# Kernel optimization log

Hardware: AMD Instinct MI355X
Metric: run time of the kernel (lower is better)

## Reference

```python
import jax, jax.numpy as jnp
import numpy as np

B, S, F_DIM, FILT = 4096, 41, 128, 128
EPS_BN = 1e-5
EPS_SQ = 1e-21


def squash(v):
    n = jnp.linalg.norm(v, axis=-1, keepdims=True)
    return (1.0 - 1.0 / (jnp.exp(n) + EPS_SQ)) * (v / (n + EPS_SQ))


def position_linear(x, Wstack, bstack, window):
    # x: [B,S,F]; Wstack: [S, window*F, FILT]; bstack: [S, FILT]
    p = window // 2
    Bq, Sq, Fq = x.shape
    xp = jnp.pad(x, ((0, 0), (p, p), (0, 0)))
    idx = jnp.arange(Sq)[:, None] + jnp.arange(window)[None, :]  # [S, window]
    xw = xp[:, idx, :].reshape(Bq, Sq, window * Fq)
    return jax.nn.relu(jnp.einsum('bsf,sfo->bso', xw, Wstack) + bstack[None])


def batchnorm(x, g, b, axes):
    mu = jnp.mean(x, axis=axes, keepdims=True)
    var = jnp.var(x, axis=axes, keepdims=True)
    shape = [1] * x.ndim
    shape[1] = x.shape[1]
    return (x - mu) * jax.lax.rsqrt(var + EPS_BN) * g.reshape(shape) + b.reshape(shape)


def conv1d(x, w, groups=1):
    # x: [N,C,L], w: [O, C//groups, K], padding same (k=3, pad=1)
    return jax.lax.conv_general_dilated(
        x, w, window_strides=(1,), padding=[(1, 1)],
        dimension_numbers=('NCH', 'OIH', 'NCH'), feature_group_count=groups)


def setup_inputs() -> dict:
    key = jax.random.key(0)
    ks = jax.random.split(key, 16)
    sc = lambda fan_in: 1.0 / np.sqrt(fan_in)
    d = {}
    d['x'] = jax.random.randint(ks[0], (B, S), 0, 4, dtype=jnp.int32)
    d['emb'] = jax.random.normal(ks[1], (4, F_DIM), dtype=jnp.float32)
    for i, w in enumerate([3, 5, 7]):
        fin = w * F_DIM
        d[f'W{w}'] = jax.random.uniform(ks[2 + i], (S, fin, FILT), jnp.float32, -sc(fin), sc(fin))
        d[f'b{w}'] = jnp.zeros((S, FILT), jnp.float32)
    d['conv1_w'] = jax.random.uniform(ks[5], (64, 41, 3), jnp.float32, -sc(41 * 3), sc(41 * 3))
    d['conv1_b'] = jnp.zeros((64,), jnp.float32)
    d['bn_g'] = jnp.ones((64,), jnp.float32)
    d['bn_b'] = jnp.zeros((64,), jnp.float32)
    d['caps_w'] = jax.random.uniform(ks[6], (64, 32, 3), jnp.float32, -sc(32 * 3), sc(32 * 3))
    d['caps_b'] = jnp.zeros((64,), jnp.float32)
    d['route_W'] = jax.random.normal(ks[7], (2, 64, F_DIM), jnp.float32)
    d['route_b'] = jnp.zeros((2, 64, 1), jnp.float32)
    d['fc1_w'] = jax.random.uniform(ks[8], (F_DIM, 64), jnp.float32, -sc(F_DIM), sc(F_DIM))
    d['bn1_g'] = jnp.ones((2,), jnp.float32)
    d['bn1_b'] = jnp.zeros((2,), jnp.float32)
    d['fc2_w'] = jax.random.uniform(ks[9], (64, 32), jnp.float32, -sc(64), sc(64))
    d['bn2_g'] = jnp.ones((2,), jnp.float32)
    d['bn2_b'] = jnp.zeros((2,), jnp.float32)
    d['fc3_w'] = jax.random.uniform(ks[10], (32, 1), jnp.float32, -sc(32), sc(32))
    return d


def reference(x, emb, W3, b3, W5, b5, W7, b7, conv1_w, conv1_b, bn_g, bn_b,
              caps_w, caps_b, route_W, route_b,
              fc1_w, bn1_g, bn1_b, fc2_w, bn2_g, bn2_b, fc3_w):
    h = emb[x]                                    # [B,41,128]
    h = position_linear(h, W3, b3, 3)
    h = position_linear(h, W5, b5, 5)
    h = position_linear(h, W7, b7, 7)             # [B,41,128]
    h = conv1d(h, conv1_w) + conv1_b[None, :, None]  # [B,64,128]
    h = jax.nn.relu(batchnorm(h, bn_g, bn_b, axes=(0, 2)))
    h = conv1d(h, caps_w, groups=2) + caps_b[None, :, None]
    h = squash(h)                                 # [B,64,128]
    # Routing layer
    u = h[:, None, :, :] * route_W[None]          # [B,2,64,128]
    c = jnp.sum(u * u, axis=-1, keepdims=True) / jnp.sqrt(128.0)  # [B,2,64,1]
    c = jax.nn.softmax(c, axis=-1)                # softmax over size-1 axis -> ones
    c = c + route_b[None]
    s = squash(jnp.sum(u * c, axis=-2))           # [B,2,128]
    # FC head
    pair = s[:, :, None, :] + s[:, None, :, :]    # [B,2,2,128]
    y = jnp.max(pair, axis=1)                     # [B,2,128]
    y = jax.nn.relu(batchnorm(y @ fc1_w, bn1_g, bn1_b, axes=(0, 2)))
    y = jax.nn.relu(batchnorm(y @ fc2_w, bn2_g, bn2_b, axes=(0, 2)))
    y = jax.nn.sigmoid(y @ fc3_w)                 # [B,2,1]
    return jnp.max(y, axis=1)                     # [B,1]
```

## Files before the change

### kernel.cpp

```cpp
#include <hip/hip_runtime.h>
#include <cstdint>

typedef unsigned short u16;
typedef unsigned int   u32;
typedef __attribute__((ext_vector_type(8))) short bf16x8;
typedef __attribute__((ext_vector_type(4))) float f32x4;

#define DEVFN static __device__ __forceinline__

constexpr int B  = 4096;
constexpr int SQ = 41;

DEVFN float bf2f(u16 v) { return __uint_as_float(((u32)v) << 16); }
DEVFN u16 f2bf(float f) {
  u32 u = __float_as_uint(f);
  u += 0x7fffu + ((u >> 16) & 1u);
  return (u16)(u >> 16);
}
DEVFN u32 pack2(float a, float b) { return (u32)f2bf(a) | ((u32)f2bf(b) << 16); }

DEVFN void gload16(const void* g, void* l) {
  __builtin_amdgcn_global_load_lds(
      (const __attribute__((address_space(1))) unsigned int*)g,
      (__attribute__((address_space(3))) unsigned int*)l, 16, 0, 0);
}

__global__ void k_pack(const float* __restrict__ cw, const float* __restrict__ cpw,
                       const float* __restrict__ rW, const float* __restrict__ rb,
                       u16* __restrict__ wpk, u16* __restrict__ cpk,
                       u16* __restrict__ rwp) {
  int i = blockIdx.x * 256 + threadIdx.x;
  if (i < 12288) {
    int tt = i >> 12, rem = i & 4095, o = rem >> 6, c = rem & 63;
    float v = (c < 41) ? cw[(o * 41 + c) * 3 + tt] : 0.f;
    wpk[(tt * 64 + o) * 64 + (c ^ ((o & 7) << 3))] = f2bf(v);
  } else if (i < 18432) {
    int k = i - 12288;
    int tt = k >> 11, rem = k & 2047, o = rem >> 5, c = rem & 31;
    cpk[(tt * 64 + o) * 32 + (c ^ ((o & 3) << 3))] = f2bf(cpw[(o * 32 + c) * 3 + tt]);
  } else if (i < 34816) {
    int k = i - 18432;
    rwp[k] = f2bf(rW[k] * (1.f + rb[k >> 7]));
  }
}

__global__ void k_combo(const int* __restrict__ x, int* __restrict__ combo) {
  int i = blockIdx.x * 256 + threadIdx.x;
  if (i >= B * SQ) return;
  int b = i / SQ, s = i - b * SQ;
  const int* xb = x + b * SQ;
  int d0 = (s > 0) ? xb[s - 1] : 4;
  int d1 = xb[s];
  int d2 = (s < SQ - 1) ? xb[s + 1] : 4;
  combo[i] = d0 * 25 + d1 * 5 + d2;
}

__global__ void k_gmat(const float* __restrict__ emb, const float* __restrict__ W3,
                       float* __restrict__ G) {
  int s = blockIdx.x / 3, ww = blockIdx.x % 3;
  int o = threadIdx.x;
  const float* Ws = W3 + ((size_t)s * 384 + ww * 128) * 128;
  float a0 = 0.f, a1 = 0.f, a2 = 0.f, a3 = 0.f;
  for (int f = 0; f < 128; ++f) {
    float wg = Ws[(size_t)f * 128 + o];
    a0 = fmaf(emb[f], wg, a0);
    a1 = fmaf(emb[128 + f], wg, a1);
    a2 = fmaf(emb[256 + f], wg, a2);
    a3 = fmaf(emb[384 + f], wg, a3);
  }
  float* Gp = G + ((size_t)(s * 3 + ww) * 5) * 128 + o;
  Gp[0] = a0; Gp[128] = a1; Gp[256] = a2; Gp[384] = a3; Gp[512] = 0.f;
}

__global__ void k_t1(const float* __restrict__ G, const float* __restrict__ b3,
                     float* __restrict__ t1T) {
  int i = blockIdx.x * 256 + threadIdx.x;
  if (i >= SQ * 128 * 125) return;
  int v = i % 125, so = i / 125;
  int s = so >> 7, o = so & 127;
  int d0 = v / 25, r = v % 25;
  int d1 = r / 5, d2 = r % 5;
  float acc = b3[so]
      + G[((size_t)(s * 3 + 0) * 5 + d0) * 128 + o]
      + G[((size_t)(s * 3 + 1) * 5 + d1) * 128 + o]
      + G[((size_t)(s * 3 + 2) * 5 + d2) * 128 + o];
  t1T[i] = fmaxf(acc, 0.f);
}

__global__ __launch_bounds__(128) void k_t2(const float* __restrict__ t1T,
                                            const float* __restrict__ W5,
                                            u16* __restrict__ t2) {
  int bx = blockIdx.x;
  int s = bx / 25; int r = bx % 25;
  int ww = r / 5;  int vt = (r % 5) * 25;
  int o = threadIdx.x;
  int t = s + ww - 2;
  u16* dst = t2 + ((size_t)(s * 5 + ww) * 125 + vt) * 128 + o;
  if (t < 0 || t >= SQ) {
    #pragma unroll
    for (int v = 0; v < 25; ++v) dst[(size_t)v * 128] = 0;
    return;
  }
  float acc[25];
  #pragma unroll
  for (int v = 0; v < 25; ++v) acc[v] = 0.f;
  const float* Ws = W5 + ((size_t)s * 640 + ww * 128) * 128;
  const float* tp = t1T + (size_t)t * 128 * 125 + vt;
  for (int f = 0; f < 128; ++f) {
    float wg = Ws[(size_t)f * 128 + o];
    #pragma unroll
    for (int v = 0; v < 25; ++v) acc[v] = fmaf(tp[f * 125 + v], wg, acc[v]);
  }
  #pragma unroll
  for (int v = 0; v < 25; ++v) dst[(size_t)v * 128] = f2bf(acc[v]);
}

__global__ __launch_bounds__(256) void k_h2(const u16* __restrict__ t2,
                                            const int* __restrict__ combo,
                                            const float* __restrict__ b5,
                                            u16* __restrict__ h2) {
  const int i = blockIdx.x * 256 + threadIdx.x;
  const int o8 = (i & 15) * 8;
  const int rid = i >> 4;
  const int s = rid >> 12, b = rid & 4095;
  float acc[8];
  {
    float4 b0 = *reinterpret_cast<const float4*>(b5 + s * 128 + o8);
    float4 b1 = *reinterpret_cast<const float4*>(b5 + s * 128 + o8 + 4);
    acc[0] = b0.x; acc[1] = b0.y; acc[2] = b0.z; acc[3] = b0.w;
    acc[4] = b1.x; acc[5] = b1.y; acc[6] = b1.z; acc[7] = b1.w;
  }
  const int* cb = combo + b * SQ;
  #pragma unroll
  for (int ww = 0; ww < 5; ++ww) {
    const int t = s + ww - 2;
    if (0 <= t && t < SQ) {
      const int c = cb[t];
      uint4 raw = *reinterpret_cast<const uint4*>(
          t2 + ((size_t)(s * 5 + ww) * 125 + c) * 128 + o8);
      acc[0] += __uint_as_float(raw.x << 16);
      acc[1] += __uint_as_float(raw.x & 0xffff0000u);
      acc[2] += __uint_as_float(raw.y << 16);
      acc[3] += __uint_as_float(raw.y & 0xffff0000u);
      acc[4] += __uint_as_float(raw.z << 16);
      acc[5] += __uint_as_float(raw.z & 0xffff0000u);
      acc[6] += __uint_as_float(raw.w << 16);
      acc[7] += __uint_as_float(raw.w & 0xffff0000u);
    }
  }
  uint4 pk;
  pk.x = pack2(fmaxf(acc[0], 0.f), fmaxf(acc[1], 0.f));
  pk.y = pack2(fmaxf(acc[2], 0.f), fmaxf(acc[3], 0.f));
  pk.z = pack2(fmaxf(acc[4], 0.f), fmaxf(acc[5], 0.f));
  pk.w = pack2(fmaxf(acc[6], 0.f), fmaxf(acc[7], 0.f));
  *reinterpret_cast<uint4*>(h2 + ((size_t)b * SQ + s) * 128 + o8) = pk;
}

__global__ __launch_bounds__(256) void k_w7t(const float* __restrict__ W7,
                                             u16* __restrict__ w7t) {
  __shared__ float tile[64][65];
  const int s = blockIdx.z;
  const int k0 = blockIdx.x * 64;
  const int o0 = blockIdx.y * 64;
  const int t = threadIdx.x;
  #pragma unroll
  for (int i = 0; i < 16; ++i) {
    int idx = t + i * 256;
    int kl = idx >> 6, ol = idx & 63;
    tile[kl][ol] = W7[((size_t)s * 896 + k0 + kl) * 128 + o0 + ol];
  }
  __syncthreads();
  #pragma unroll
  for (int i = 0; i < 16; ++i) {
    int idx = t + i * 256;
    int ol = idx >> 6, kl = idx & 63;
    w7t[((size_t)s * 128 + o0 + ol) * 896 + k0 + kl] = f2bf(tile[kl][ol]);
  }
}

__global__ __launch_bounds__(256) void k_gemm7_mfma(const u16* __restrict__ h2,
                                                    const u16* __restrict__ w7t,
                                                    const float* __restrict__ b7,
                                                    u16* __restrict__ h3) {
  __shared__ u16 As[2][8192];
  __shared__ u16 Bs[2][8192];
  const int s  = blockIdx.y;
  const int b0 = blockIdx.x * 128;
  const int t  = threadIdx.x;
  const int lane = t & 63, w = t >> 6;
  const int wr = w >> 1, wc = w & 1;
  const int lcol = lane & 15, qk = lane >> 4;

  f32x4 acc[4][4];
  #pragma unroll
  for (int i = 0; i < 4; ++i)
    #pragma unroll
    for (int j = 0; j < 4; ++j) acc[i][j] = (f32x4){0.f, 0.f, 0.f, 0.f};

  const u16* wbase = w7t + (size_t)s * 128 * 896;

  auto stage = [&](int kt, int bi) -> int {
    const int k0 = kt * 64;
    const int ww = k0 >> 7, tr = s + ww - 3, kf0 = k0 & 127;
    int issued = 0;
    if (0 <= tr && tr < SQ) {
      #pragma unroll
      for (int it = 0; it < 4; ++it) {
        const int L = it * 4096 + t * 16;
        const int r = L >> 7;
        const int g = (L >> 4) & 7;
        const int gs = g ^ (r & 7);
        gload16(h2 + ((size_t)(b0 + r) * SQ + tr) * 128 + kf0 + gs * 8,
                (char*)As[bi] + it * 4096 + w * 1024);
      }
      issued += 4;
    } else {
      #pragma unroll
      for (int it = 0; it < 4; ++it)
        *reinterpret_cast<uint4*>((char*)As[bi] + it * 4096 + t * 16) =
            make_uint4(0u, 0u, 0u, 0u);
    }
    #pragma unroll
    for (int it = 0; it < 4; ++it) {
      const int L = it * 4096 + t * 16;
      const int o = L >> 7;
      const int g = (L >> 4) & 7;
      const int gs = g ^ (o & 7);
      gload16(wbase + (size_t)o * 896 + k0 + gs * 8,
              (char*)Bs[bi] + it * 4096 + w * 1024);
    }
    return issued + 4;
  };

  stage(0, 0);

  for (int kt = 0; kt < 14; ++kt) {
    const int cur = kt & 1;
    int ni = 0;
    if (kt < 13) ni = stage(kt + 1, cur ^ 1);
    if (ni == 8)      asm volatile("s_waitcnt vmcnt(8) lgkmcnt(0)" ::: "memory");
    else if (ni == 4) asm volatile("s_waitcnt vmcnt(4) lgkmcnt(0)" ::: "memory");
    else              asm volatile("s_waitcnt vmcnt(0) lgkmcnt(0)" ::: "memory");
    __builtin_amdgcn_sched_barrier(0);
    __builtin_amdgcn_s_barrier();
    __builtin_amdgcn_sched_barrier(0);

    const u16* Ac = As[cur];
    const u16* Bc = Bs[cur];
    #pragma unroll
    for (int kk = 0; kk < 2; ++kk) {
      const int gk = kk * 4 + qk;
      bf16x8 av[4], bv[4];
      #pragma unroll
      for (int m = 0; m < 4; ++m) {
        const int zr = wr * 64 + m * 16 + lcol;
        av[m] = *reinterpret_cast<const bf16x8*>(Ac + zr * 64 + ((gk ^ (zr & 7)) << 3));
      }
      #pragma unroll
      for (int n = 0; n < 4; ++n) {
        const int br = wc * 64 + n * 16 + lcol;
        bv[n] = *reinterpret_cast<const bf16x8*>(Bc + br * 64 + ((gk ^ (br & 7)) << 3));
      }
      #pragma unroll
      for (int m = 0; m < 4; ++m)
        #pragma unroll
        for (int n = 0; n < 4; ++n)
          acc[m][n] = __builtin_amdgcn_mfma_f32_16x16x32_bf16(av[m], bv[n], acc[m][n], 0, 0, 0);
    }
    __builtin_amdgcn_sched_barrier(0);
    __builtin_amdgcn_s_barrier();
  }

  const int rq = (lane >> 4) * 4;
  #pragma unroll
  for (int n = 0; n < 4; ++n) {
    const int o = wc * 64 + n * 16 + lcol;
    const float bias = b7[s * 128 + o];
    #pragma unroll
    for (int m = 0; m < 4; ++m) {
      #pragma unroll
      for (int rg = 0; rg < 4; ++rg) {
        const int row = b0 + wr * 64 + m * 16 + rq + rg;
        h3[((size_t)row * SQ + s) * 128 + o] = f2bf(fmaxf(acc[m][n][rg] + bias, 0.f));
      }
    }
  }
}

__global__ __launch_bounds__(256) void k_conv1(const u16* __restrict__ h3,
                                               const u16* __restrict__ wpk,
                                               const float* __restrict__ cb,
                                               u16* __restrict__ c1T,
                                               float2* __restrict__ part) {
  __shared__ u16 zs[6144];
  __shared__ u16 zt[130 * 64];
  __shared__ u16 wl[3 * 64 * 64];
  __shared__ float2 red[4][64];
  const int b = blockIdx.x;
  const int t = threadIdx.x;
  const int lane = t & 63, wv = t >> 6;

  const u16* src = h3 + (size_t)b * (SQ * 128);
  #pragma unroll
  for (int it = 0; it < 3; ++it)
    gload16(src + ((size_t)it * 256 + t) * 8, (char*)zs + it * 4096 + wv * 1024);
  #pragma unroll
  for (int it = 0; it < 6; ++it)
    gload16(wpk + ((size_t)it * 256 + t) * 8, (char*)wl + it * 4096 + wv * 1024);

  if (t < 64) zt[t] = 0;
  else if (t < 128) zt[129 * 64 + t - 64] = 0;
  __syncthreads();

  {
    const int l = t & 127, jb = (t >> 7) * 32;
    const int sw = ((l + 1) & 7) << 3;
    u16* dst = zt + (l + 1) * 64;
    #pragma unroll
    for (int j = 0; j < 32; ++j) {
      int c = (jb + j + l) & 63;
      dst[c ^ sw] = (c < 41) ? zs[c * 128 + l] : (u16)0;
    }
  }
  __syncthreads();

  f32x4 acc[2][4];
  #pragma unroll
  for (int m = 0; m < 2; ++m)
    #pragma unroll
    for (int n = 0; n < 4; ++n) acc[m][n] = (f32x4){0.f, 0.f, 0.f, 0.f};
  const int r = lane & 15, kq = (lane >> 4) * 8;

  #pragma unroll
  for (int tt = 0; tt < 3; ++tt) {
    #pragma unroll
    for (int kk = 0; kk < 2; ++kk) {
      const int kof = kk * 32 + kq;
      bf16x8 av[2], bv[4];
      #pragma unroll
      for (int m = 0; m < 2; ++m) {
        const int zr = wv * 32 + m * 16 + r + tt;
        av[m] = *reinterpret_cast<const bf16x8*>(zt + zr * 64 + (kof ^ ((zr & 7) << 3)));
      }
      #pragma unroll
      for (int n = 0; n < 4; ++n) {
        const int o = n * 16 + r;
        bv[n] = *reinterpret_cast<const bf16x8*>(wl + (tt * 64 + o) * 64 + (kof ^ ((o & 7) << 3)));
      }
      #pragma unroll
      for (int m = 0; m < 2; ++m)
        #pragma unroll
        for (int n = 0; n < 4; ++n)
          acc[m][n] = __builtin_amdgcn_mfma_f32_16x16x32_bf16(av[m], bv[n], acc[m][n], 0, 0, 0);
    }
  }

  const int q = lane >> 4;
  u16* outb = c1T + (size_t)b * 8192;
  #pragma unroll
  for (int n = 0; n < 4; ++n) {
    const int o = n * 16 + r;
    const float bias = cb[o];
    float s1 = 0.f, s2 = 0.f;
    #pragma unroll
    for (int m = 0; m < 2; ++m) {
      #pragma unroll
      for (int rg = 0; rg < 4; ++rg) {
        float v = acc[m][n][rg] + bias;
        s1 += v; s2 += v * v;
        outb[(wv * 32 + m * 16 + q * 4 + rg) * 64 + o] = f2bf(v);
      }
    }
    s1 += __shfl_xor(s1, 16); s1 += __shfl_xor(s1, 32);
    s2 += __shfl_xor(s2, 16); s2 += __shfl_xor(s2, 32);
    if (lane < 16) red[wv][n * 16 + lane] = make_float2(s1, s2);
  }
  __syncthreads();
  if (t < 64) {
    float S = red[0][t].x + red[1][t].x + red[2][t].x + red[3][t].x;
    float Q = red[0][t].y + red[1][t].y + red[2][t].y + red[3][t].y;
    part[(size_t)t * B + b] = make_float2(S, Q);
  }
}

__global__ void k_bnfin(const float2* __restrict__ part, const float* __restrict__ g,
                        const float* __restrict__ bb, float* __restrict__ scale,
                        float* __restrict__ shift) {
  int o = blockIdx.x;
  float s = 0.f, q = 0.f;
  for (int i = threadIdx.x; i < B; i += 256) {
    float2 p = part[(size_t)o * B + i];
    s += p.x; q += p.y;
  }
  #pragma unroll
  for (int off = 32; off; off >>= 1) { s += __shfl_down(s, off); q += __shfl_down(q, off); }
  __shared__ float rs[4], rq[4];
  int wv = threadIdx.x >> 6, ln = threadIdx.x & 63;
  if (ln == 0) { rs[wv] = s; rq[wv] = q; }
  __syncthreads();
  if (threadIdx.x == 0) {
    float S = rs[0] + rs[1] + rs[2] + rs[3];
    float Q = rq[0] + rq[1] + rq[2] + rq[3];
    const float n = (float)B * 128.f;
    float mu = S / n, var = Q / n - mu * mu;
    float sc = g[o] * rsqrtf(var + 1e-5f);
    scale[o] = sc; shift[o] = bb[o] - mu * sc;
  }
}

constexpr int NB = 8;
__global__ __launch_bounds__(256) void k_caps(const u16* __restrict__ c1T,
                                              const float* __restrict__ scale,
                                              const float* __restrict__ shift,
                                              const u16* __restrict__ cpk,
                                              const float* __restrict__ cpb,
                                              const u16* __restrict__ rwp,
                                              const float* __restrict__ f1,
                                              float* __restrict__ y1) {
  __shared__ u16 zt[130 * 64];
  __shared__ u16 wl[3 * 64 * 32];
  __shared__ float f1l[128 * 64];
  __shared__ float red[4][64];
  __shared__ float fl[64];
  __shared__ float sc_s[64], sh_s[64];
  __shared__ float red2[4][2];
  __shared__ float yl[2][128];
  __shared__ float pt[128];
  const int b0 = blockIdx.x * NB;
  const int t = threadIdx.x;
  const int lane = t & 63, wv = t >> 6;
  const int r = lane & 15, kq = (lane >> 4) * 8, q = lane >> 4;

  #pragma unroll
  for (int it = 0; it < 3; ++it)
    gload16(cpk + ((size_t)it * 256 + t) * 8, (char*)wl + it * 4096 + wv * 1024);
  #pragma unroll
  for (int it = 0; it < 8; ++it)
    gload16(f1 + ((size_t)it * 256 + t) * 4, (char*)f1l + it * 4096 + wv * 1024);
  if (t < 64) { sc_s[t] = scale[t]; sh_s[t] = shift[t]; }
  if (t < 64) zt[t] = 0;
  else if (t < 128) zt[129 * 64 + t - 64] = 0;

  uint4 raw[4], rawn[4];
  {
    const u16* src = c1T + (size_t)b0 * 8192;
    #pragma unroll
    for (int p = 0; p < 4; ++p)
      raw[p] = *reinterpret_cast<const uint4*>(src + ((size_t)t + p * 256) * 8);
  }

  for (int i = 0; i < NB; ++i) {
    const int b = b0 + i;
    __syncthreads();

    #pragma unroll
    for (int p = 0; p < 4; ++p) {
      int idx = t + p * 256;
      int l = idx >> 3, c0 = (idx & 7) * 8;
      float vv[8];
      vv[0] = __uint_as_float(raw[p].x << 16); vv[1] = __uint_as_float(raw[p].x & 0xffff0000u);
      vv[2] = __uint_as_float(raw[p].y << 16); vv[3] = __uint_as_float(raw[p].y & 0xffff0000u);
      vv[4] = __uint_as_float(raw[p].z << 16); vv[5] = __uint_as_float(raw[p].z & 0xffff0000u);
      vv[6] = __uint_as_float(raw[p].w << 16); vv[7] = __uint_as_float(raw[p].w & 0xffff0000u);
      float a0 = fmaxf(fmaf(vv[0], sc_s[c0 + 0], sh_s[c0 + 0]), 0.f);
      float a1 = fmaxf(fmaf(vv[1], sc_s[c0 + 1], sh_s[c0 + 1]), 0.f);
      float a2 = fmaxf(fmaf(vv[2], sc_s[c0 + 2], sh_s[c0 + 2]), 0.f);
      float a3 = fmaxf(fmaf(vv[3], sc_s[c0 + 3], sh_s[c0 + 3]), 0.f);
      float a4 = fmaxf(fmaf(vv[4], sc_s[c0 + 4], sh_s[c0 + 4]), 0.f);
      float a5 = fmaxf(fmaf(vv[5], sc_s[c0 + 5], sh_s[c0 + 5]), 0.f);
      float a6 = fmaxf(fmaf(vv[6], sc_s[c0 + 6], sh_s[c0 + 6]), 0.f);
      float a7 = fmaxf(fmaf(vv[7], sc_s[c0 + 7], sh_s[c0 + 7]), 0.f);
      uint4 pk;
      pk.x = pack2(a0, a1); pk.y = pack2(a2, a3);
      pk.z = pack2(a4, a5); pk.w = pack2(a6, a7);
      *reinterpret_cast<uint4*>(zt + (l + 1) * 64 + (c0 ^ (((l + 1) & 7) << 3))) = pk;
    }
    if (i + 1 < NB) {
      const u16* srcn = c1T + (size_t)(b + 1) * 8192;
      #pragma unroll
      for (int p = 0; p < 4; ++p)
        rawn[p] = *reinterpret_cast<const uint4*>(srcn + ((size_t)t + p * 256) * 8);
    }
    __syncthreads();

    f32x4 acc[2][4];
    #pragma unroll
    for (int m = 0; m < 2; ++m)
      #pragma unroll
      for (int n = 0; n < 4; ++n) acc[m][n] = (f32x4){0.f, 0.f, 0.f, 0.f};
    #pragma unroll
    for (int tt = 0; tt < 3; ++tt) {
      bf16x8 av[2][2], bv[4];
      #pragma unroll
      for (int m = 0; m < 2; ++m) {
        const int zr = wv * 32 + m * 16 + r + tt;
        const int sw = (zr & 7) << 3;
        av[m][0] = *reinterpret_cast<const bf16x8*>(zt + zr * 64 + (kq ^ sw));
        av[m][1] = *reinterpret_cast<const bf16x8*>(zt + zr * 64 + ((32 + kq) ^ sw));
      }
      #pragma unroll
      for (int n = 0; n < 4; ++n) {
        const int o = n * 16 + r;
        bv[n] = *reinterpret_cast<const bf16x8*>(wl + (tt * 64 + o) * 32 + (kq ^ ((o & 3) << 3)));
      }
      #pragma unroll
      for (int m = 0; m < 2; ++m)
        #pragma unroll
        for (int n = 0; n < 4; ++n)
          acc[m][n] = __builtin_amdgcn_mfma_f32_16x16x32_bf16(av[m][n >> 1], bv[n], acc[m][n], 0, 0, 0);
    }

    #pragma unroll
    for (int n = 0; n < 4; ++n) {
      const int o = n * 16 + r;
      const float bias = cpb[o];
      float s2 = 0.f;
      #pragma unroll
      for (int m = 0; m < 2; ++m) {
        #pragma unroll
        for (int rg = 0; rg < 4; ++rg) {
          float v = acc[m][n][rg] + bias;
          acc[m][n][rg] = v;
          s2 += v * v;
        }
      }
      s2 += __shfl_xor(s2, 16); s2 += __shfl_xor(s2, 32);
      if (lane < 16) red[wv][n * 16 + lane] = s2;
    }
    __syncthreads();
    if (t < 64) {
      float S = red[0][t] + red[1][t] + red[2][t] + red[3][t];
      float nn = sqrtf(S);
      fl[t] = (1.f - 1.f / (expf(nn) + 1e-21f)) / (nn + 1e-21f);
    }
    __syncthreads();

    float s0[2][4], s1[2][4];
    #pragma unroll
    for (int m = 0; m < 2; ++m)
      #pragma unroll
      for (int rg = 0; rg < 4; ++rg) { s0[m][rg] = 0.f; s1[m][rg] = 0.f; }
    #pragma unroll
    for (int n = 0; n < 4; ++n) {
      const int o = n * 16 + r;
      const float fact = fl[o];
      #pragma unroll
      for (int m = 0; m < 2; ++m) {
        const int l0 = wv * 32 + m * 16 + q * 4;
        uint2 rw0 = *reinterpret_cast<const uint2*>(rwp + (size_t)o * 128 + l0);
        uint2 rw1 = *reinterpret_cast<const uint2*>(rwp + (size_t)(64 + o) * 128 + l0);
        #pragma unroll
        for (int rg = 0; rg < 4; ++rg) {
          float v = acc[m][n][rg] * fact;
          u32 w0w = (rg < 2) ? rw0.x : rw0.y;
          u32 w1w = (rg < 2) ? rw1.x : rw1.y;
          float w0 = __uint_as_float((rg & 1) ? (w0w & 0xffff0000u) : (w0w << 16));
          float w1 = __uint_as_float((rg & 1) ? (w1w & 0xffff0000u) : (w1w << 16));
          s0[m][rg] = fmaf(v, w0, s0[m][rg]);
          s1[m][rg] = fmaf(v, w1, s1[m][rg]);
        }
      }
    }
    #pragma unroll
    for (int m = 0; m < 2; ++m)
      #pragma unroll
      for (int rg = 0; rg < 4; ++rg) {
        #pragma unroll
        for (int off = 1; off <= 8; off <<= 1) {
          s0[m][rg] += __shfl_xor(s0[m][rg], off);
          s1[m][rg] += __shfl_xor(s1[m][rg], off);
        }
      }
    float n0 = 0.f, n1 = 0.f;
    #pragma unroll
    for (int m = 0; m < 2; ++m)
      #pragma unroll
      for (int rg = 0; rg < 4; ++rg) {
        n0 = fmaf(s0[m][rg], s0[m][rg], n0);
        n1 = fmaf(s1[m][rg], s1[m][rg], n1);
      }
    n0 += __shfl_xor(n0, 16); n0 += __shfl_xor(n0, 32);
    n1 += __shfl_xor(n1, 16); n1 += __shfl_xor(n1, 32);
    if (lane == 0) { red2[wv][0] = n0; red2[wv][1] = n1; }
    __syncthreads();
    {
      float t0 = red2[0][0] + red2[1][0] + red2[2][0] + red2[3][0];
      float t1 = red2[0][1] + red2[1][1] + red2[2][1] + red2[3][1];
      float nn0 = sqrtf(t0), nn1 = sqrtf(t1);
      float fa0 = (1.f - 1.f / (expf(nn0) + 1e-21f)) / (nn0 + 1e-21f);
      float fa1 = (1.f - 1.f / (expf(nn1) + 1e-21f)) / (nn1 + 1e-21f);
      if (r == 0) {
        #pragma unroll
        for (int m = 0; m < 2; ++m)
          #pragma unroll
          for (int rg = 0; rg < 4; ++rg) {
            float v0 = s0[m][rg] * fa0, v1 = s1[m][rg] * fa1;
            float mx = fmaxf(v0, v1);
            int l = wv * 32 + m * 16 + q * 4 + rg;
            yl[0][l] = v0 + mx;
            yl[1][l] = v1 + mx;
          }
      }
    }
    __syncthreads();

    {
      const int h = t >> 7, idx = t & 127;
      const int jj = idx >> 6, qq = idx & 63;
      float a = 0.f;
      const float* yrow = &yl[jj][h * 64];
      const float* frow = f1l + (h * 64) * 64 + qq;
      #pragma unroll 8
      for (int tt = 0; tt < 64; ++tt)
        a = fmaf(yrow[tt], frow[tt * 64], a);
      if (h == 1) pt[idx] = a;
      __syncthreads();
      if (h == 0)
        y1[((size_t)b * 2 + jj) * 64 + qq] = a + pt[idx];
    }

    #pragma unroll
    for (int p = 0; p < 4; ++p) raw[p] = rawn[p];
  }
}

__global__ __launch_bounds__(256) void k_bnstat_part(const float* __restrict__ y,
                                                     float2* __restrict__ pp,
                                                     int perShift) {
  const int jj = blockIdx.y;
  const int per = 1 << perShift;
  const int n4 = (B << perShift) >> 2;
  const int p4shift = perShift - 2;
  const int p4mask = (per >> 2) - 1;
  float s = 0.f, q = 0.f;
  for (int i = blockIdx.x * 256 + threadIdx.x; i < n4; i += 64 * 256) {
    int bI = i >> p4shift, c4 = (i & p4mask) * 4;
    float4 v = *reinterpret_cast<const float4*>(
        y + (size_t)bI * (per * 2) + jj * per + c4);
    s += v.x + v.y + v.z + v.w;
    q += v.x * v.x + v.y * v.y + v.z * v.z + v.w * v.w;
  }
  #pragma unroll
  for (int off = 32; off; off >>= 1) { s += __shfl_down(s, off); q += __shfl_down(q, off); }
  __shared__ float rs[4], rq[4];
  int wv = threadIdx.x >> 6, ln = threadIdx.x & 63;
  if (ln == 0) { rs[wv] = s; rq[wv] = q; }
  __syncthreads();
  if (threadIdx.x == 0)
    pp[jj * 64 + blockIdx.x] =
        make_float2(rs[0] + rs[1] + rs[2] + rs[3], rq[0] + rq[1] + rq[2] + rq[3]);
}

__global__ void k_bnstat_fin(const float2* __restrict__ pp, const float* __restrict__ g,
                             const float* __restrict__ bb, float* __restrict__ scale,
                             float* __restrict__ shift, int perShift) {
  const int jj = blockIdx.x;
  float2 p = pp[jj * 64 + threadIdx.x];
  float s = p.x, q = p.y;
  #pragma unroll
  for (int off = 32; off; off >>= 1) { s += __shfl_down(s, off); q += __shfl_down(q, off); }
  if (threadIdx.x == 0) {
    float fn = (float)(B << perShift);
    float mu = s / fn, var = q / fn - mu * mu;
    float sc = g[jj] * rsqrtf(var + 1e-5f);
    scale[jj] = sc; shift[jj] = bb[jj] - mu * sc;
  }
}

__global__ void k_fc2(const float* __restrict__ y1, const float* __restrict__ sc1,
                      const float* __restrict__ sh1, const float* __restrict__ f2,
                      float* __restrict__ y2) {
  int t = threadIdx.x;
  int b = blockIdx.x * 4 + (t >> 6);
  int jj = (t >> 5) & 1, r = t & 31;
  float sc = sc1[jj], sh = sh1[jj];
  const float* yb = y1 + (size_t)b * 128 + jj * 64;
  float acc = 0.f;
  for (int q = 0; q < 64; ++q) {
    float v = fmaxf(fmaf(yb[q], sc, sh), 0.f);
    acc = fmaf(v, f2[q * 32 + r], acc);
  }
  y2[(size_t)b * 64 + jj * 32 + r] = acc;
}

__global__ void k_head(const float* __restrict__ y2, const float* __restrict__ sc2,
                       const float* __restrict__ sh2, const float* __restrict__ f3,
                       float* __restrict__ out) {
  int b = blockIdx.x * 256 + threadIdx.x;
  if (b >= B) return;
  const float* yb = y2 + (size_t)b * 64;
  float c0 = sc2[0], d0 = sh2[0], c1v = sc2[1], d1 = sh2[1];
  float a0 = 0.f, a1 = 0.f;
  for (int r = 0; r < 32; ++r) {
    float w = f3[r];
    a0 = fmaf(fmaxf(fmaf(yb[r], c0, d0), 0.f), w, a0);
    a1 = fmaf(fmaxf(fmaf(yb[32 + r], c1v, d1), 0.f), w, a1);
  }
  float s0 = 1.f / (1.f + expf(-a0));
  float s1 = 1.f / (1.f + expf(-a1));
  out[b] = fmaxf(s0, s1);
}

constexpr size_t SZ_H2    = (size_t)B * SQ * 128 * 2;
constexpr size_t SZ_C1    = (size_t)B * 64 * 128 * 2;
constexpr size_t OFF_H2   = 0;
constexpr size_t OFF_H3   = SZ_H2;
constexpr size_t R1       = 2 * SZ_H2;
constexpr size_t OFF_G    = R1;
constexpr size_t OFF_T1   = OFF_G + 314880;
constexpr size_t OFF_T2   = OFF_T1 + 2624000;
constexpr size_t OFF_CMB  = OFF_T2 + 6560000;
constexpr size_t OFF_W7T  = OFF_CMB + 671744;
constexpr size_t OFF_C1   = R1;
constexpr size_t R2       = R1 + SZ_C1;
constexpr size_t OFF_PART = R2;
constexpr size_t OFF_Y1   = OFF_PART + 2097152;
constexpr size_t OFF_Y2   = OFF_Y1 + 2097152;
constexpr size_t OFF_SM   = OFF_Y2 + 1048576;
constexpr size_t OFF_BNP  = OFF_SM + 1024;
constexpr size_t OFF_WPK  = OFF_BNP + 1024;
constexpr size_t OFF_CPK  = OFF_WPK + 24576;
constexpr size_t OFF_RWP  = OFF_CPK + 12288;

extern "C" void kernel_launch(void* const* d_in, const int* in_sizes, int n_in,
                              void* d_out, int out_size, void* d_ws, size_t ws_size,
                              hipStream_t stream) {
  const int*   x   = (const int*)d_in[0];
  const float* emb = (const float*)d_in[1];
  const float* W3  = (const float*)d_in[2];
  const float* b3  = (const float*)d_in[3];
  const float* W5  = (const float*)d_in[4];
  const float* b5  = (const float*)d_in[5];
  const float* W7  = (const float*)d_in[6];
  const float* b7  = (const float*)d_in[7];
  const float* c1w = (const float*)d_in[8];
  const float* c1b = (const float*)d_in[9];
  const float* bng = (const float*)d_in[10];
  const float* bnb = (const float*)d_in[11];
  const float* cpw = (const float*)d_in[12];
  const float* cpb = (const float*)d_in[13];
  const float* rW  = (const float*)d_in[14];
  const float* rb  = (const float*)d_in[15];
  const float* f1  = (const float*)d_in[16];
  const float* g1  = (const float*)d_in[17];
  const float* bb1 = (const float*)d_in[18];
  const float* f2  = (const float*)d_in[19];
  const float* g2  = (const float*)d_in[20];
  const float* bb2 = (const float*)d_in[21];
  const float* f3  = (const float*)d_in[22];

  char* wsb = (char*)d_ws;
  u16*    h2p   = (u16*)(wsb + OFF_H2);
  u16*    h3p   = (u16*)(wsb + OFF_H3);
  float*  Gp    = (float*)(wsb + OFF_G);
  float*  t1p   = (float*)(wsb + OFF_T1);
  u16*    t2p   = (u16*)(wsb + OFF_T2);
  int*    cmbp  = (int*)(wsb + OFF_CMB);
  u16*    w7tp  = (u16*)(wsb + OFF_W7T);
  u16*    c1p   = (u16*)(wsb + OFF_C1);
  float2* partp = (float2*)(wsb + OFF_PART);
  float*  y1p   = (float*)(wsb + OFF_Y1);
  float*  y2p   = (float*)(wsb + OFF_Y2);
  float*  scp   = (float*)(wsb + OFF_SM);
  float*  shp   = scp + 64;
  float*  sc1p  = shp + 64;
  float*  sh1p  = sc1p + 2;
  float*  sc2p  = sh1p + 2;
  float*  sh2p  = sc2p + 2;
  float2* bnpp  = (float2*)(wsb + OFF_BNP);
  u16*    wpkp  = (u16*)(wsb + OFF_WPK);
  u16*    cpkp  = (u16*)(wsb + OFF_CPK);
  u16*    rwpp  = (u16*)(wsb + OFF_RWP);

  k_pack<<<136, 256, 0, stream>>>(c1w, cpw, rW, rb, wpkp, cpkp, rwpp);
  k_combo<<<(B * SQ + 255) / 256, 256, 0, stream>>>(x, cmbp);
  k_w7t<<<dim3(14, 2, SQ), 256, 0, stream>>>(W7, w7tp);
  k_gmat<<<SQ * 3, 128, 0, stream>>>(emb, W3, Gp);
  k_t1<<<(SQ * 128 * 125 + 255) / 256, 256, 0, stream>>>(Gp, b3, t1p);
  k_t2<<<SQ * 25, 128, 0, stream>>>(t1p, W5, t2p);
  k_h2<<<(B * SQ * 16) / 256, 256, 0, stream>>>(t2p, cmbp, b5, h2p);
  k_gemm7_mfma<<<dim3(32, SQ), 256, 0, stream>>>(h2p, w7tp, b7, h3p);
  k_conv1<<<B, 256, 0, stream>>>(h3p, wpkp, c1b, c1p, partp);
  k_bnfin<<<64, 256, 0, stream>>>(partp, bng, bnb, scp, shp);
  k_caps<<<B / NB, 256, 0, stream>>>(c1p, scp, shp, cpkp, cpb, rwpp, f1, y1p);
  k_bnstat_part<<<dim3(64, 2), 256, 0, stream>>>(y1p, bnpp, 6);
  k_bnstat_fin<<<2, 64, 0, stream>>>(bnpp, g1, bb1, sc1p, sh1p, 6);
  k_fc2<<<B / 4, 256, 0, stream>>>(y1p, sc1p, sh1p, f2, y2p);
  k_bnstat_part<<<dim3(64, 2), 256, 0, stream>>>(y2p, bnpp, 5);
  k_bnstat_fin<<<2, 64, 0, stream>>>(bnpp, g2, bb2, sc2p, sh2p, 5);
  k_head<<<B / 256, 256, 0, stream>>>(y2p, sc2p, sh2p, f3, (float*)d_out);
}
```

Baseline: 244.2 us.

## Process eight batch rows per conv1 block with double-buffered input prefetch

Each k_conv1 block now handles eight consecutive batch elements instead of one. The packed conv weights are loaded into LDS once and reused for all eight, instead of being reloaded per batch element. The next element's input tile is prefetched into a second LDS buffer while the current one is transposed and multiplied. This cuts redundant weight traffic and per-block setup, but the grid shrinks to 512 blocks and each block holds more LDS, which lowers parallelism and adds two barriers per iteration.

```diff
diff --git a/kernel.cpp b/kernel.cpp
--- a/kernel.cpp
+++ b/kernel.cpp
@@ -287,99 +287,113 @@
   }
 }
 
+constexpr int NBC = 8;
 __global__ __launch_bounds__(256) void k_conv1(const u16* __restrict__ h3,
                                                const u16* __restrict__ wpk,
                                                const float* __restrict__ cb,
                                                u16* __restrict__ c1T,
                                                float2* __restrict__ part) {
-  __shared__ u16 zs[6144];
+  __shared__ u16 zs[2][6144];
   __shared__ u16 zt[130 * 64];
   __shared__ u16 wl[3 * 64 * 64];
   __shared__ float2 red[4][64];
-  const int b = blockIdx.x;
+  const int b0 = blockIdx.x * NBC;
   const int t = threadIdx.x;
   const int lane = t & 63, wv = t >> 6;
-
-  const u16* src = h3 + (size_t)b * (SQ * 128);
-  #pragma unroll
-  for (int it = 0; it < 3; ++it)
-    gload16(src + ((size_t)it * 256 + t) * 8, (char*)zs + it * 4096 + wv * 1024);
+  const int r = lane & 15, kq = (lane >> 4) * 8, q = lane >> 4;
+
   #pragma unroll
   for (int it = 0; it < 6; ++it)
     gload16(wpk + ((size_t)it * 256 + t) * 8, (char*)wl + it * 4096 + wv * 1024);
-
+  #pragma unroll
+  for (int it = 0; it < 3; ++it)
+    gload16(h3 + (size_t)b0 * (SQ * 128) + ((size_t)it * 256 + t) * 8,
+            (char*)zs[0] + it * 4096 + wv * 1024);
   if (t < 64) zt[t] = 0;
   else if (t < 128) zt[129 * 64 + t - 64] = 0;
   __syncthreads();
 
-  {
-    const int l = t & 127, jb = (t >> 7) * 32;
-    const int sw = ((l + 1) & 7) << 3;
-    u16* dst = zt + (l + 1) * 64;
-    #pragma unroll
-    for (int j = 0; j < 32; ++j) {
-      int c = (jb + j + l) & 63;
-      dst[c ^ sw] = (c < 41) ? zs[c * 128 + l] : (u16)0;
-    }
-  }
-  __syncthreads();
-
-  f32x4 acc[2][4];
-  #pragma unroll
-  for (int m = 0; m < 2; ++m)
-    #pragma unroll
-    for (int n = 0; n < 4; ++n) acc[m][n] = (f32x4){0.f, 0.f, 0.f, 0.f};
-  const int r = lane & 15, kq = (lane >> 4) * 8;
-
-  #pragma unroll
-  for (int tt = 0; tt < 3; ++tt) {
-    #pragma unroll
-    for (int kk = 0; kk < 2; ++kk) {
-      const int kof = kk * 32 + kq;
-      bf16x8 av[2], bv[4];
+  for (int i = 0; i < NBC; ++i) {
+    const int b = b0 + i;
+    const int cur = i & 1;
+
+    {
+      const int l = t & 127, jb = (t >> 7) * 32;
+      const int sw = ((l + 1) & 7) << 3;
+      u16* dst = zt + (l + 1) * 64;
+      const u16* srcz = zs[cur];
+      #pragma unroll
+      for (int j = 0; j < 32; ++j) {
+        int c = (jb + j + l) & 63;
+        dst[c ^ sw] = (c < 41) ? srcz[c * 128 + l] : (u16)0;
+      }
+    }
+    if (i + 1 < NBC) {
+      #pragma unroll
+      for (int it = 0; it < 3; ++it)
+        gload16(h3 + (size_t)(b + 1) * (SQ * 128) + ((size_t)it * 256 + t) * 8,
+                (char*)zs[cur ^ 1] + it * 4096 + wv * 1024);
+    }
+    asm volatile("s_waitcnt lgkmcnt(0)" ::: "memory");
+    __builtin_amdgcn_sched_barrier(0);
+    __builtin_amdgcn_s_barrier();
+    __builtin_amdgcn_sched_barrier(0);
+
+    f32x4 acc[2][4];
+    #pragma unroll
+    for (int m = 0; m < 2; ++m)
+      #pragma unroll
+      for (int n = 0; n < 4; ++n) acc[m][n] = (f32x4){0.f, 0.f, 0.f, 0.f};
+    #pragma unroll
+    for (int tt = 0; tt < 3; ++tt) {
+      #pragma unroll
+      for (int kk = 0; kk < 2; ++kk) {
+        const int kof = kk * 32 + kq;
+        bf16x8 av[2], bv[4];
+        #pragma unroll
+        for (int m = 0; m < 2; ++m) {
+          const int zr = wv * 32 + m * 16 + r + tt;
+          av[m] = *reinterpret_cast<const bf16x8*>(zt + zr * 64 + (kof ^ ((zr & 7) << 3)));
+        }
+        #pragma unroll
+        for (int n = 0; n < 4; ++n) {
+          const int o = n * 16 + r;
+          bv[n] = *reinterpret_cast<const bf16x8*>(wl + (tt * 64 + o) * 64 + (kof ^ ((o & 7) << 3)));
+        }
+        #pragma unroll
+        for (int m = 0; m < 2; ++m)
+          #pragma unroll
+          for (int n = 0; n < 4; ++n)
+            acc[m][n] = __builtin_amdgcn_mfma_f32_16x16x32_bf16(av[m], bv[n], acc[m][n], 0, 0, 0);
+      }
+    }
+
+    u16* outb = c1T + (size_t)b * 8192;
+    #pragma unroll
+    for (int n = 0; n < 4; ++n) {
+      const int o = n * 16 + r;
+      const float bias = cb[o];
+      float s1 = 0.f, s2 = 0.f;
       #pragma unroll
       for (int m = 0; m < 2; ++m) {
-        const int zr = wv * 32 + m * 16 + r + tt;
-        av[m] = *reinterpret_cast<const bf16x8*>(zt + zr * 64 + (kof ^ ((zr & 7) << 3)));
-      }
-      #pragma unroll
-      for (int n = 0; n < 4; ++n) {
-        const int o = n * 16 + r;
-        bv[n] = *reinterpret_cast<const bf16x8*>(wl + (tt * 64 + o) * 64 + (kof ^ ((o & 7) << 3)));
-      }
-      #pragma unroll
-      for (int m = 0; m < 2; ++m)
-        #pragma unroll
-        for (int n = 0; n < 4; ++n)
-          acc[m][n] = __builtin_amdgcn_mfma_f32_16x16x32_bf16(av[m], bv[n], acc[m][n], 0, 0, 0);
-    }
-  }
-
-  const int q = lane >> 4;
-  u16* outb = c1T + (size_t)b * 8192;
-  #pragma unroll
-  for (int n = 0; n < 4; ++n) {
-    const int o = n * 16 + r;
-    const float bias = cb[o];
-    float s1 = 0.f, s2 = 0.f;
-    #pragma unroll
-    for (int m = 0; m < 2; ++m) {
-      #pragma unroll
-      for (int rg = 0; rg < 4; ++rg) {
-        float v = acc[m][n][rg] + bias;
-        s1 += v; s2 += v * v;
-        outb[(wv * 32 + m * 16 + q * 4 + rg) * 64 + o] = f2bf(v);
-      }
-    }
-    s1 += __shfl_xor(s1, 16); s1 += __shfl_xor(s1, 32);
-    s2 += __shfl_xor(s2, 16); s2 += __shfl_xor(s2, 32);
-    if (lane < 16) red[wv][n * 16 + lane] = make_float2(s1, s2);
-  }
-  __syncthreads();
-  if (t < 64) {
-    float S = red[0][t].x + red[1][t].x + red[2][t].x + red[3][t].x;
-    float Q = red[0][t].y + red[1][t].y + red[2][t].y + red[3][t].y;
-    part[(size_t)t * B + b] = make_float2(S, Q);
+        #pragma unroll
+        for (int rg = 0; rg < 4; ++rg) {
+          float v = acc[m][n][rg] + bias;
+          s1 += v; s2 += v * v;
+          outb[(wv * 32 + m * 16 + q * 4 + rg) * 64 + o] = f2bf(v);
+        }
+      }
+      s1 += __shfl_xor(s1, 16); s1 += __shfl_xor(s1, 32);
+      s2 += __shfl_xor(s2, 16); s2 += __shfl_xor(s2, 32);
+      if (lane < 16) red[wv][n * 16 + lane] = make_float2(s1, s2);
+    }
+    __syncthreads();
+    if (t < 64) {
+      float S = red[0][t].x + red[1][t].x + red[2][t].x + red[3][t].x;
+      float Q = red[0][t].y + red[1][t].y + red[2][t].y + red[3][t].y;
+      part[(size_t)t * B + b] = make_float2(S, Q);
+    }
+    __syncthreads();
   }
 }
 
@@ -780,7 +794,7 @@
   k_t2<<<SQ * 25, 128, 0, stream>>>(t1p, W5, t2p);
   k_h2<<<(B * SQ * 16) / 256, 256, 0, stream>>>(t2p, cmbp, b5, h2p);
   k_gemm7_mfma<<<dim3(32, SQ), 256, 0, stream>>>(h2p, w7tp, b7, h3p);
-  k_conv1<<<B, 256, 0, stream>>>(h3p, wpkp, c1b, c1p, partp);
+  k_conv1<<<B / NBC, 256, 0, stream>>>(h3p, wpkp, c1b, c1p, partp);
   k_bnfin<<<64, 256, 0, stream>>>(partp, bng, bnb, scp, shp);
   k_caps<<<B / NB, 256, 0, stream>>>(c1p, scp, shp, cpkp, cpb, rwpp, f1, y1p);
   k_bnstat_part<<<dim3(64, 2), 256, 0, stream>>>(y1p, bnpp, 6);
```

Result: faster. 236.0 us (-3.3%).
